# Optimization experiments

Hardware: AMD Instinct MI355X
Metric: run time of the kernel (lower is better)

Reference implementation:

```python
import jax, jax.numpy as jnp
import numpy as np

C = 128
IC = C // 2  # inter_channels
EPS = 1e-5   # InstanceNorm2d default eps (affine=False -> no learned scale/shift)


def setup_inputs() -> dict:
    key = jax.random.key(0)
    ks = jax.random.split(key, 9)
    s = 0.05
    return {
        "x": jax.random.normal(ks[0], (4, C, 64, 64), dtype=jnp.float32),
        "g_w": jax.random.normal(ks[1], (IC, C), dtype=jnp.float32) * s,
        "g_b": jax.random.normal(ks[2], (IC,), dtype=jnp.float32) * s,
        "theta_w": jax.random.normal(ks[3], (IC, C), dtype=jnp.float32) * s,
        "theta_b": jax.random.normal(ks[4], (IC,), dtype=jnp.float32) * s,
        "phi_w": jax.random.normal(ks[5], (IC, C), dtype=jnp.float32) * s,
        "phi_b": jax.random.normal(ks[6], (IC,), dtype=jnp.float32) * s,
        "W_w": jax.random.normal(ks[7], (C, IC), dtype=jnp.float32) * s,
        "W_b": jax.random.normal(ks[8], (C,), dtype=jnp.float32) * s,
    }


def reference(x, g_w, g_b, theta_w, theta_b, phi_w, phi_b, W_w, W_b):
    B, Cc, H, Wd = x.shape
    N = H * Wd
    xf = x.reshape(B, Cc, N)  # [B, C, N]

    def proj(w, b):  # 1x1 conv == channel matmul
        return jnp.einsum('oc,bcn->bon', w, xf) + b[:, None]  # [B, IC, N]

    g_x = proj(g_w, g_b).transpose(0, 2, 1)        # [B, N, IC]
    theta_x = proj(theta_w, theta_b).transpose(0, 2, 1)  # [B, N, IC]
    phi_x = proj(phi_w, phi_b)                     # [B, IC, N]

    f = jnp.einsum('bnc,bcm->bnm', theta_x, phi_x)  # [B, N, N] unscaled affinity
    f = jax.nn.softmax(f, axis=-1)
    y = jnp.einsum('bnm,bmc->bnc', f, g_x)          # [B, N, IC]
    y = y.transpose(0, 2, 1)                        # [B, IC, N]

    W_y = jnp.einsum('oc,bcn->bon', W_w, y) + W_b[:, None]  # [B, C, N]
    # InstanceNorm2d (affine=False): normalize per (batch, channel) over spatial
    mean = W_y.mean(axis=-1, keepdims=True)
    var = W_y.var(axis=-1, keepdims=True)
    W_y = (W_y - mean) * jax.lax.rsqrt(var + EPS)

    return x + W_y.reshape(B, Cc, H, Wd)
```

## Files before the change

### kernel.cpp

```cpp
#include <hip/hip_runtime.h>
#include <math.h>

typedef __attribute__((ext_vector_type(4))) float f32x4;
typedef __attribute__((ext_vector_type(8))) short s16x8;
typedef __attribute__((ext_vector_type(4))) short s16x4;
typedef __attribute__((ext_vector_type(4))) unsigned int u32x4;

#define NB 4
#define CH 128
#define ICH 64
#define NSP 4096
#define KSPLIT 16
#define SEGK (NSP / KSPLIT)
#define LDK 72
#define LDW 136

static __device__ __forceinline__ unsigned short f2bf(float f) {
  unsigned int u = __builtin_bit_cast(unsigned int, f);
  u += 0x7fffu + ((u >> 16) & 1u);
  return (unsigned short)(u >> 16);
}

__global__ __launch_bounds__(256) void k_proj(
    const float* __restrict__ x,
    const float* __restrict__ gw, const float* __restrict__ gbias,
    const float* __restrict__ tw, const float* __restrict__ tbias,
    const float* __restrict__ pw, const float* __restrict__ pbias,
    unsigned short* __restrict__ thetaT, unsigned short* __restrict__ phiT,
    unsigned short* __restrict__ gout)
{
  __shared__ __align__(16) float sxf[CH * 65];
  __shared__ __align__(16) unsigned short sW[ICH * LDW];
  const int b = blockIdx.y, z = blockIdx.z;
  const int n0 = blockIdx.x * 64;
  const int t = threadIdx.x;
  const float* Wz = (z == 0) ? tw : (z == 1) ? pw : gw;
  const float* Bz = (z == 0) ? tbias : (z == 1) ? pbias : gbias;
  const float scl = (z == 0) ? 1.44269504f : 1.0f;
  const float* xb = x + (size_t)b * CH * NSP;
#pragma unroll
  for (int i = 0; i < 8; ++i) {
    int idx = t + 256 * i;
    int c = idx >> 4, ch = idx & 15;
    *(float4*)(sxf + c * 65 + ch * 4) = *(const float4*)(xb + (size_t)c * NSP + n0 + ch * 4);
  }
#pragma unroll
  for (int i = 0; i < 8; ++i) {
    int idx = t + 256 * i;
    int o = idx >> 5, col = (idx & 31) * 4;
    float4 wv = *(const float4*)(Wz + o * CH + col);
    unsigned int p0 = (unsigned int)f2bf(wv.x) | ((unsigned int)f2bf(wv.y) << 16);
    unsigned int p1 = (unsigned int)f2bf(wv.z) | ((unsigned int)f2bf(wv.w) << 16);
    *(unsigned int*)(&sW[o * LDW + col]) = p0;
    *(unsigned int*)(&sW[o * LDW + col + 2]) = p1;
  }
  __syncthreads();

  const int wave = t >> 6, lane = t & 63;
  const int l15 = lane & 15, quad = lane >> 4;
  const int nw = wave * 16;
  s16x8 aq[4];
#pragma unroll
  for (int kc = 0; kc < 4; ++kc) {
#pragma unroll
    for (int j = 0; j < 8; ++j)
      aq[kc][j] = (short)f2bf(sxf[(kc * 32 + quad * 8 + j) * 65 + nw + l15]);
  }
  __syncthreads();

  unsigned short* ldsT = (unsigned short*)sxf;

#pragma unroll
  for (int osub = 0; osub < 4; ++osub) {
    f32x4 acc = (f32x4){0.f, 0.f, 0.f, 0.f};
#pragma unroll
    for (int kc = 0; kc < 4; ++kc) {
      const unsigned short* wp = &sW[(osub * 16 + l15) * LDW + kc * 32 + quad * 8];
      s16x4 lo = *(const s16x4*)(wp);
      s16x4 hi = *(const s16x4*)(wp + 4);
      s16x8 bw = __builtin_shufflevector(lo, hi, 0, 1, 2, 3, 4, 5, 6, 7);
      acc = __builtin_amdgcn_mfma_f32_16x16x32_bf16(aq[kc], bw, acc, 0, 0, 0);
    }
    float bv = Bz[osub * 16 + l15];
    if (z < 2) {
      unsigned short* outp = (z == 0) ? thetaT : phiT;
#pragma unroll
      for (int r = 0; r < 4; ++r)
        outp[((size_t)b * NSP + n0 + nw + quad * 4 + r) * ICH + osub * 16 + l15] =
            f2bf((acc[r] + bv) * scl);
    } else {
#pragma unroll
      for (int r = 0; r < 4; ++r)
        ldsT[(nw + quad * 4 + r) * LDK + osub * 16 + l15] = f2bf(acc[r] + bv);
    }
  }
  if (z == 2) {
    __syncthreads();
    int o = t >> 2, chunk = t & 3;
    unsigned short vv[16];
#pragma unroll
    for (int jj = 0; jj < 16; ++jj) vv[jj] = ldsT[(chunk * 16 + jj) * LDK + o];
    unsigned int words[8];
#pragma unroll
    for (int i = 0; i < 8; ++i)
      words[i] = (unsigned int)vv[2 * i] | ((unsigned int)vv[2 * i + 1] << 16);
    unsigned short* gp = gout + ((size_t)b * ICH + o) * NSP + n0 + chunk * 16;
    *(u32x4*)(gp) = (u32x4){words[0], words[1], words[2], words[3]};
    *(u32x4*)(gp + 8) = (u32x4){words[4], words[5], words[6], words[7]};
  }
}

__global__ __launch_bounds__(256, 2) void k_attn(
    const unsigned short* __restrict__ thetaT,
    const unsigned short* __restrict__ phiT,
    const unsigned short* __restrict__ gmat,
    unsigned short* __restrict__ Opart, float* __restrict__ lpart)
{
  __shared__ unsigned short ldsK[64 * LDK];
  __shared__ unsigned short ldsV[64 * LDK];
  __shared__ unsigned short ldsP[4][16 * LDK];
  const int qt = blockIdx.x, b = blockIdx.y, seg = blockIdx.z;
  const int t = threadIdx.x;
  const int wave = t >> 6, lane = t & 63;
  const int l15 = lane & 15, quad = lane >> 4;
  const int q0 = qt * 256 + wave * 64;

  s16x8 aq[4][2];
  const unsigned short* th = thetaT + ((size_t)b * NSP + q0) * ICH;
#pragma unroll
  for (int qs = 0; qs < 4; ++qs)
#pragma unroll
    for (int ks = 0; ks < 2; ++ks)
      aq[qs][ks] = __builtin_bit_cast(s16x8,
          *(const u32x4*)(th + (qs * 16 + l15) * ICH + ks * 32 + quad * 8));

  f32x4 Oacc[4][4];
  f32x4 lacc[4];
#pragma unroll
  for (int i = 0; i < 4; ++i) {
    lacc[i] = (f32x4){0.f, 0.f, 0.f, 0.f};
#pragma unroll
    for (int j = 0; j < 4; ++j) Oacc[i][j] = (f32x4){0.f, 0.f, 0.f, 0.f};
  }

  s16x8 bones;
  {
    short v = (l15 == 0) ? (short)0x3F80 : (short)0;
#pragma unroll
    for (int j = 0; j < 8; ++j) bones[j] = v;
  }

  const unsigned short* ph = phiT + (size_t)b * NSP * ICH;
  const unsigned short* gb = gmat + (size_t)b * ICH * NSP;
  const int k0 = seg * SEGK;

  for (int kt = 0; kt < SEGK / 64; ++kt) {
    const int key0 = k0 + kt * 64;
    __syncthreads();
#pragma unroll
    for (int i = 0; i < 4; ++i) {
      int idx = t + 256 * i;
      int rr = (idx >> 3) & 63, c8 = (idx & 7) * 8;
      if (idx < 512)
        *(u32x4*)(&ldsK[rr * LDK + c8]) =
            *(const u32x4*)(ph + (size_t)(key0 + rr) * ICH + c8);
      else
        *(u32x4*)(&ldsV[rr * LDK + c8]) =
            *(const u32x4*)(gb + (size_t)rr * NSP + key0 + c8);
    }
    __syncthreads();

    s16x8 bk[4][2];
#pragma unroll
    for (int kc = 0; kc < 4; ++kc)
#pragma unroll
      for (int ks = 0; ks < 2; ++ks)
        bk[kc][ks] = *(const s16x8*)(&ldsK[(kc * 16 + l15) * LDK + ks * 32 + quad * 8]);
    s16x8 bv[2][4];
#pragma unroll
    for (int ks = 0; ks < 2; ++ks)
#pragma unroll
      for (int ds = 0; ds < 4; ++ds)
        bv[ks][ds] = *(const s16x8*)(&ldsV[(ds * 16 + l15) * LDK + ks * 32 + quad * 8]);

    unsigned short* myP = &ldsP[wave][0];
#pragma unroll
    for (int qs = 0; qs < 4; ++qs) {
#pragma unroll
      for (int kc = 0; kc < 4; ++kc) {
        f32x4 sacc = (f32x4){0.f, 0.f, 0.f, 0.f};
        sacc = __builtin_amdgcn_mfma_f32_16x16x32_bf16(aq[qs][0], bk[kc][0], sacc, 0, 0, 0);
        sacc = __builtin_amdgcn_mfma_f32_16x16x32_bf16(aq[qs][1], bk[kc][1], sacc, 0, 0, 0);
#pragma unroll
        for (int r = 0; r < 4; ++r) {
          float e = exp2f(sacc[r]);
          myP[(quad * 4 + r) * LDK + kc * 16 + l15] =
              (unsigned short)(__builtin_bit_cast(unsigned int, e) >> 16);
        }
      }
#pragma unroll
      for (int ks = 0; ks < 2; ++ks) {
        s16x8 ap = *(const s16x8*)(&myP[l15 * LDK + ks * 32 + quad * 8]);
        lacc[qs] = __builtin_amdgcn_mfma_f32_16x16x32_bf16(ap, bones, lacc[qs], 0, 0, 0);
#pragma unroll
        for (int ds = 0; ds < 4; ++ds)
          Oacc[qs][ds] = __builtin_amdgcn_mfma_f32_16x16x32_bf16(ap, bv[ks][ds], Oacc[qs][ds], 0, 0, 0);
      }
    }
  }

  unsigned short* Ob = Opart + (((size_t)seg * NB + b) * NSP + q0) * ICH;
  unsigned short* myP = &ldsP[wave][0];
  const int erow = lane >> 3;
  const int ecol = (lane & 7) * 8;
#pragma unroll
  for (int qs = 0; qs < 4; ++qs) {
#pragma unroll
    for (int ds = 0; ds < 4; ++ds)
#pragma unroll
      for (int r = 0; r < 4; ++r)
        myP[(quad * 4 + r) * LDK + ds * 16 + l15] = f2bf(Oacc[qs][ds][r]);
    u32x4 w0 = *(const u32x4*)(&myP[erow * LDK + ecol]);
    u32x4 w1 = *(const u32x4*)(&myP[(8 + erow) * LDK + ecol]);
    *(u32x4*)(Ob + (qs * 16 + erow) * ICH + ecol) = w0;
    *(u32x4*)(Ob + (qs * 16 + 8 + erow) * ICH + ecol) = w1;
  }
  {
    float* myPf = (float*)myP;
    if (l15 == 0) {
#pragma unroll
      for (int qs = 0; qs < 4; ++qs)
#pragma unroll
        for (int r = 0; r < 4; ++r)
          myPf[qs * 16 + quad * 4 + r] = lacc[qs][r];
    }
    float* lb = lpart + ((size_t)seg * NB + b) * NSP + q0;
    lb[lane] = myPf[lane];
  }
}

__global__ __launch_bounds__(128) void k_wy(
    const unsigned short* __restrict__ Opart, const float* __restrict__ lpart,
    const float* __restrict__ Ww,
    float* __restrict__ WyT, float* __restrict__ stat)
{
  const int b = blockIdx.y, nt = blockIdx.x;
  const int t = threadIdx.x;
  const int wave = t >> 6, lane = t & 63;
  const int l15 = lane & 15, quad = lane >> 4;
  const int n0 = nt * 32 + wave * 16;
  float ls = 0.f;
#pragma unroll
  for (int s = 0; s < KSPLIT; ++s)
    ls += lpart[((size_t)s * NB + b) * NSP + n0 + l15];
  float inv = 1.0f / ls;
  s16x8 ay[2];
#pragma unroll
  for (int ks = 0; ks < 2; ++ks) {
    float acc8[8];
#pragma unroll
    for (int j = 0; j < 8; ++j) acc8[j] = 0.f;
#pragma unroll
    for (int s = 0; s < KSPLIT; ++s) {
      const unsigned short* op =
          Opart + (((size_t)s * NB + b) * NSP + n0 + l15) * ICH + ks * 32 + quad * 8;
      u32x4 raw = *(const u32x4*)op;
#pragma unroll
      for (int w2 = 0; w2 < 4; ++w2) {
        unsigned int u = raw[w2];
        acc8[2 * w2]     += __builtin_bit_cast(float, u << 16);
        acc8[2 * w2 + 1] += __builtin_bit_cast(float, u & 0xFFFF0000u);
      }
    }
#pragma unroll
    for (int j = 0; j < 8; ++j) ay[ks][j] = (short)f2bf(acc8[j] * inv);
  }
  s16x8 bw[8][2];
#pragma unroll
  for (int cc = 0; cc < 8; ++cc)
#pragma unroll
    for (int ks = 0; ks < 2; ++ks) {
      const float* wp = Ww + (cc * 16 + l15) * ICH + ks * 32 + quad * 8;
      s16x8 e;
#pragma unroll
      for (int j = 0; j < 8; ++j) e[j] = (short)f2bf(wp[j]);
      bw[cc][ks] = e;
    }
  float sums[8], sq[8];
#pragma unroll
  for (int cc = 0; cc < 8; ++cc) { sums[cc] = 0.f; sq[cc] = 0.f; }
#pragma unroll
  for (int cc = 0; cc < 8; ++cc) {
    f32x4 acc = (f32x4){0.f, 0.f, 0.f, 0.f};
    acc = __builtin_amdgcn_mfma_f32_16x16x32_bf16(ay[0], bw[cc][0], acc, 0, 0, 0);
    acc = __builtin_amdgcn_mfma_f32_16x16x32_bf16(ay[1], bw[cc][1], acc, 0, 0, 0);
    float* wout = WyT + ((size_t)b * NSP + n0 + quad * 4) * CH + cc * 16 + l15;
#pragma unroll
    for (int r = 0; r < 4; ++r) {
      float v = acc[r];
      sums[cc] += v;
      sq[cc] += v * v;
      wout[r * CH] = v;
    }
  }
#pragma unroll
  for (int cc = 0; cc < 8; ++cc) {
    sums[cc] += __shfl_xor(sums[cc], 16, 64);
    sums[cc] += __shfl_xor(sums[cc], 32, 64);
    sq[cc] += __shfl_xor(sq[cc], 16, 64);
    sq[cc] += __shfl_xor(sq[cc], 32, 64);
  }
  if (quad == 0) {
#pragma unroll
    for (int cc = 0; cc < 8; ++cc) {
      atomicAdd(&stat[(b * CH + cc * 16 + l15) * 2 + 0], sums[cc]);
      atomicAdd(&stat[(b * CH + cc * 16 + l15) * 2 + 1], sq[cc]);
    }
  }
}

__global__ __launch_bounds__(256) void k_norm(
    const float* __restrict__ WyT, const float* __restrict__ stat,
    const float* __restrict__ x, float* __restrict__ out)
{
  __shared__ float sWy[32 * 132];
  const int nt = blockIdx.x;
  const int b = blockIdx.y;
  const int t = threadIdx.x;
  const int n0 = nt * 32;
#pragma unroll
  for (int i = 0; i < 4; ++i) {
    int idx = t + 256 * i;
    int row = idx >> 5, c4 = idx & 31;
    *(float4*)(&sWy[row * 132 + c4 * 4]) =
        *(const float4*)(WyT + ((size_t)b * NSP + n0 + row) * CH + c4 * 4);
  }
  __syncthreads();
#pragma unroll
  for (int j = 0; j < 4; ++j) {
    int u = t + 256 * j;
    int co = u >> 3, nq = u & 7;
    float s = stat[(b * CH + co) * 2 + 0];
    float ss = stat[(b * CH + co) * 2 + 1];
    float mean = s * (1.f / NSP);
    float var = ss * (1.f / NSP) - mean * mean;
    float rs = rsqrtf(var + 1e-5f);
    float4 xv = *(const float4*)(x + (size_t)(b * CH + co) * NSP + n0 + nq * 4);
    float4 ov;
    ov.x = xv.x + (sWy[(nq * 4 + 0) * 132 + co] - mean) * rs;
    ov.y = xv.y + (sWy[(nq * 4 + 1) * 132 + co] - mean) * rs;
    ov.z = xv.z + (sWy[(nq * 4 + 2) * 132 + co] - mean) * rs;
    ov.w = xv.w + (sWy[(nq * 4 + 3) * 132 + co] - mean) * rs;
    *(float4*)(out + (size_t)(b * CH + co) * NSP + n0 + nq * 4) = ov;
  }
}

extern "C" void kernel_launch(void* const* d_in, const int* in_sizes, int n_in,
                              void* d_out, int out_size, void* d_ws, size_t ws_size,
                              hipStream_t stream)
{
  const float* x  = (const float*)d_in[0];
  const float* gw = (const float*)d_in[1];
  const float* gb = (const float*)d_in[2];
  const float* tw = (const float*)d_in[3];
  const float* tb = (const float*)d_in[4];
  const float* pw = (const float*)d_in[5];
  const float* pb = (const float*)d_in[6];
  const float* Ww = (const float*)d_in[7];
  float* out = (float*)d_out;
  char* ws = (char*)d_ws;
  unsigned short* thetaT = (unsigned short*)(ws);
  unsigned short* phiT   = (unsigned short*)(ws + (2ull << 20));
  unsigned short* gmat   = (unsigned short*)(ws + (4ull << 20));
  float* WyT   = (float*)(ws + (8ull << 20));
  float* stat  = (float*)(ws + (16ull << 20));
  float* lpart = (float*)(ws + (16ull << 20) + (1ull << 18));
  unsigned short* Opart = (unsigned short*)(ws + (17ull << 20) + (1ull << 18));

  hipMemsetAsync(stat, 0, NB * CH * 2 * sizeof(float), stream);
  k_proj<<<dim3(64, 4, 3), 256, 0, stream>>>(x, gw, gb, tw, tb, pw, pb, thetaT, phiT, gmat);
  k_attn<<<dim3(16, 4, KSPLIT), 256, 0, stream>>>(thetaT, phiT, gmat, Opart, lpart);
  k_wy<<<dim3(128, 4), 128, 0, stream>>>(Opart, lpart, Ww, WyT, stat);
  k_norm<<<dim3(128, 4), 256, 0, stream>>>(WyT, stat, x, out);
}
```

Measured before the change: 147.6 us.

## Pre-convert weights to bf16 once, fuse three projections per block, halve KSPLIT

Adds a small kernel that converts all four weight matrices to bf16 once and zeroes the stat buffer, replacing the memset. k_proj now computes theta, phi and g in one block per 32-column tile, reading x once instead of three times, and writes theta/phi through LDS as coalesced 16-byte stores. k_wy reads the pre-converted bf16 W weights directly. KSPLIT drops from 16 to 8, which halves the partial-output traffic in k_wy but reduces attention grid parallelism.

```diff
diff --git a/kernel.cpp b/kernel.cpp
--- a/kernel.cpp
+++ b/kernel.cpp
@@ -3,17 +3,16 @@
 
 typedef __attribute__((ext_vector_type(4))) float f32x4;
 typedef __attribute__((ext_vector_type(8))) short s16x8;
-typedef __attribute__((ext_vector_type(4))) short s16x4;
 typedef __attribute__((ext_vector_type(4))) unsigned int u32x4;
+typedef __attribute__((ext_vector_type(2))) unsigned int u32x2;
 
 #define NB 4
 #define CH 128
 #define ICH 64
 #define NSP 4096
-#define KSPLIT 16
+#define KSPLIT 8
 #define SEGK (NSP / KSPLIT)
 #define LDK 72
-#define LDW 136
 
 static __device__ __forceinline__ unsigned short f2bf(float f) {
   unsigned int u = __builtin_bit_cast(unsigned int, f);
@@ -21,92 +20,93 @@
   return (unsigned short)(u >> 16);
 }
 
-__global__ __launch_bounds__(256) void k_proj(
+__global__ __launch_bounds__(256) void k_wconv(
+    const float* __restrict__ tw, const float* __restrict__ pw,
+    const float* __restrict__ gw, const float* __restrict__ Ww,
+    unsigned short* __restrict__ Wwb, float* __restrict__ stat)
+{
+  int i = blockIdx.x * 256 + threadIdx.x;
+  int which = i >> 11;
+  const float* src = (which == 0) ? tw : (which == 1) ? pw : (which == 2) ? gw : Ww;
+  float4 v = ((const float4*)src)[i & 2047];
+  unsigned int p0 = (unsigned int)f2bf(v.x) | ((unsigned int)f2bf(v.y) << 16);
+  unsigned int p1 = (unsigned int)f2bf(v.z) | ((unsigned int)f2bf(v.w) << 16);
+  *(u32x2*)(Wwb + i * 4) = (u32x2){p0, p1};
+  if (blockIdx.x == 0) {
+    float4 z = {0.f, 0.f, 0.f, 0.f};
+    ((float4*)stat)[threadIdx.x] = z;
+  }
+}
+
+__global__ __launch_bounds__(128) void k_proj(
     const float* __restrict__ x,
-    const float* __restrict__ gw, const float* __restrict__ gbias,
-    const float* __restrict__ tw, const float* __restrict__ tbias,
-    const float* __restrict__ pw, const float* __restrict__ pbias,
+    const float* __restrict__ gbias, const float* __restrict__ tbias,
+    const float* __restrict__ pbias,
+    const unsigned short* __restrict__ Wwb,
     unsigned short* __restrict__ thetaT, unsigned short* __restrict__ phiT,
     unsigned short* __restrict__ gout)
 {
-  __shared__ __align__(16) float sxf[CH * 65];
-  __shared__ __align__(16) unsigned short sW[ICH * LDW];
-  const int b = blockIdx.y, z = blockIdx.z;
-  const int n0 = blockIdx.x * 64;
+  __shared__ __align__(16) unsigned short ldsT[32 * LDK];
+  const int b = blockIdx.y;
+  const int n0 = blockIdx.x * 32;
   const int t = threadIdx.x;
-  const float* Wz = (z == 0) ? tw : (z == 1) ? pw : gw;
-  const float* Bz = (z == 0) ? tbias : (z == 1) ? pbias : gbias;
-  const float scl = (z == 0) ? 1.44269504f : 1.0f;
-  const float* xb = x + (size_t)b * CH * NSP;
-#pragma unroll
-  for (int i = 0; i < 8; ++i) {
-    int idx = t + 256 * i;
-    int c = idx >> 4, ch = idx & 15;
-    *(float4*)(sxf + c * 65 + ch * 4) = *(const float4*)(xb + (size_t)c * NSP + n0 + ch * 4);
-  }
-#pragma unroll
-  for (int i = 0; i < 8; ++i) {
-    int idx = t + 256 * i;
-    int o = idx >> 5, col = (idx & 31) * 4;
-    float4 wv = *(const float4*)(Wz + o * CH + col);
-    unsigned int p0 = (unsigned int)f2bf(wv.x) | ((unsigned int)f2bf(wv.y) << 16);
-    unsigned int p1 = (unsigned int)f2bf(wv.z) | ((unsigned int)f2bf(wv.w) << 16);
-    *(unsigned int*)(&sW[o * LDW + col]) = p0;
-    *(unsigned int*)(&sW[o * LDW + col + 2]) = p1;
-  }
-  __syncthreads();
-
   const int wave = t >> 6, lane = t & 63;
   const int l15 = lane & 15, quad = lane >> 4;
-  const int nw = wave * 16;
+  const int n = n0 + wave * 16 + l15;
+  const float* xb = x + (size_t)b * CH * NSP;
+
   s16x8 aq[4];
 #pragma unroll
-  for (int kc = 0; kc < 4; ++kc) {
+  for (int kc = 0; kc < 4; ++kc)
 #pragma unroll
     for (int j = 0; j < 8; ++j)
-      aq[kc][j] = (short)f2bf(sxf[(kc * 32 + quad * 8 + j) * 65 + nw + l15]);
-  }
-  __syncthreads();
-
-  unsigned short* ldsT = (unsigned short*)sxf;
-
-#pragma unroll
-  for (int osub = 0; osub < 4; ++osub) {
-    f32x4 acc = (f32x4){0.f, 0.f, 0.f, 0.f};
-#pragma unroll
-    for (int kc = 0; kc < 4; ++kc) {
-      const unsigned short* wp = &sW[(osub * 16 + l15) * LDW + kc * 32 + quad * 8];
-      s16x4 lo = *(const s16x4*)(wp);
-      s16x4 hi = *(const s16x4*)(wp + 4);
-      s16x8 bw = __builtin_shufflevector(lo, hi, 0, 1, 2, 3, 4, 5, 6, 7);
-      acc = __builtin_amdgcn_mfma_f32_16x16x32_bf16(aq[kc], bw, acc, 0, 0, 0);
-    }
-    float bv = Bz[osub * 16 + l15];
+      aq[kc][j] = (short)f2bf(xb[(size_t)(kc * 32 + quad * 8 + j) * NSP + n]);
+
+  unsigned short* myT = &ldsT[wave * 16 * LDK];
+  const int erow = lane >> 3, ecol = (lane & 7) * 8;
+
+#pragma unroll
+  for (int z = 0; z < 3; ++z) {
+    const float* Bz = (z == 0) ? tbias : (z == 1) ? pbias : gbias;
+    const float scl = (z == 0) ? 1.44269504f : 1.0f;
+    const unsigned short* Wz = Wwb + z * (ICH * CH);
+#pragma unroll
+    for (int osub = 0; osub < 4; ++osub) {
+      f32x4 acc = (f32x4){0.f, 0.f, 0.f, 0.f};
+#pragma unroll
+      for (int kc = 0; kc < 4; ++kc) {
+        s16x8 bw = __builtin_bit_cast(s16x8,
+            *(const u32x4*)(Wz + (osub * 16 + l15) * CH + kc * 32 + quad * 8));
+        acc = __builtin_amdgcn_mfma_f32_16x16x32_bf16(aq[kc], bw, acc, 0, 0, 0);
+      }
+      float bv = Bz[osub * 16 + l15];
+#pragma unroll
+      for (int r = 0; r < 4; ++r)
+        myT[(quad * 4 + r) * LDK + osub * 16 + l15] = f2bf((acc[r] + bv) * scl);
+    }
     if (z < 2) {
-      unsigned short* outp = (z == 0) ? thetaT : phiT;
-#pragma unroll
-      for (int r = 0; r < 4; ++r)
-        outp[((size_t)b * NSP + n0 + nw + quad * 4 + r) * ICH + osub * 16 + l15] =
-            f2bf((acc[r] + bv) * scl);
+      unsigned short* outp = ((z == 0) ? thetaT : phiT) + ((size_t)b * NSP + n0 + wave * 16) * ICH;
+      u32x4 w0 = *(const u32x4*)(&myT[erow * LDK + ecol]);
+      u32x4 w1 = *(const u32x4*)(&myT[(8 + erow) * LDK + ecol]);
+      *(u32x4*)(outp + erow * ICH + ecol) = w0;
+      *(u32x4*)(outp + (8 + erow) * ICH + ecol) = w1;
     } else {
-#pragma unroll
-      for (int r = 0; r < 4; ++r)
-        ldsT[(nw + quad * 4 + r) * LDK + osub * 16 + l15] = f2bf(acc[r] + bv);
-    }
-  }
-  if (z == 2) {
-    __syncthreads();
-    int o = t >> 2, chunk = t & 3;
-    unsigned short vv[16];
-#pragma unroll
-    for (int jj = 0; jj < 16; ++jj) vv[jj] = ldsT[(chunk * 16 + jj) * LDK + o];
-    unsigned int words[8];
-#pragma unroll
-    for (int i = 0; i < 8; ++i)
-      words[i] = (unsigned int)vv[2 * i] | ((unsigned int)vv[2 * i + 1] << 16);
-    unsigned short* gp = gout + ((size_t)b * ICH + o) * NSP + n0 + chunk * 16;
-    *(u32x4*)(gp) = (u32x4){words[0], words[1], words[2], words[3]};
-    *(u32x4*)(gp + 8) = (u32x4){words[4], words[5], words[6], words[7]};
+      __syncthreads();
+#pragma unroll
+      for (int jj = 0; jj < 2; ++jj) {
+        int o = (wave * 2 + jj) * 16 + (lane >> 2);
+        int nch = (lane & 3) * 8;
+        unsigned short vv[8];
+#pragma unroll
+        for (int q2 = 0; q2 < 8; ++q2) vv[q2] = ldsT[(nch + q2) * LDK + o];
+        unsigned int words[4];
+#pragma unroll
+        for (int i2 = 0; i2 < 4; ++i2)
+          words[i2] = (unsigned int)vv[2 * i2] | ((unsigned int)vv[2 * i2 + 1] << 16);
+        *(u32x4*)(gout + ((size_t)b * ICH + o) * NSP + n0 + nch) =
+            (u32x4){words[0], words[1], words[2], words[3]};
+      }
+    }
   }
 }
 
@@ -241,7 +241,7 @@
 
 __global__ __launch_bounds__(128) void k_wy(
     const unsigned short* __restrict__ Opart, const float* __restrict__ lpart,
-    const float* __restrict__ Ww,
+    const unsigned short* __restrict__ Wwb,
     float* __restrict__ WyT, float* __restrict__ stat)
 {
   const int b = blockIdx.y, nt = blockIdx.x;
@@ -275,17 +275,14 @@
 #pragma unroll
     for (int j = 0; j < 8; ++j) ay[ks][j] = (short)f2bf(acc8[j] * inv);
   }
+  const unsigned short* Wb = Wwb + 3 * (ICH * CH);
   s16x8 bw[8][2];
 #pragma unroll
   for (int cc = 0; cc < 8; ++cc)
 #pragma unroll
-    for (int ks = 0; ks < 2; ++ks) {
-      const float* wp = Ww + (cc * 16 + l15) * ICH + ks * 32 + quad * 8;
-      s16x8 e;
-#pragma unroll
-      for (int j = 0; j < 8; ++j) e[j] = (short)f2bf(wp[j]);
-      bw[cc][ks] = e;
-    }
+    for (int ks = 0; ks < 2; ++ks)
+      bw[cc][ks] = __builtin_bit_cast(s16x8,
+          *(const u32x4*)(Wb + (cc * 16 + l15) * ICH + ks * 32 + quad * 8));
   float sums[8], sq[8];
 #pragma unroll
   for (int cc = 0; cc < 8; ++cc) { sums[cc] = 0.f; sq[cc] = 0.f; }
@@ -374,12 +371,13 @@
   unsigned short* gmat   = (unsigned short*)(ws + (4ull << 20));
   float* WyT   = (float*)(ws + (8ull << 20));
   float* stat  = (float*)(ws + (16ull << 20));
-  float* lpart = (float*)(ws + (16ull << 20) + (1ull << 18));
-  unsigned short* Opart = (unsigned short*)(ws + (17ull << 20) + (1ull << 18));
-
-  hipMemsetAsync(stat, 0, NB * CH * 2 * sizeof(float), stream);
-  k_proj<<<dim3(64, 4, 3), 256, 0, stream>>>(x, gw, gb, tw, tb, pw, pb, thetaT, phiT, gmat);
+  unsigned short* Wwb = (unsigned short*)(ws + (16ull << 20) + 65536);
+  float* lpart = (float*)(ws + (16ull << 20) + (1ull << 19));
+  unsigned short* Opart = (unsigned short*)(ws + (17ull << 20));
+
+  k_wconv<<<dim3(32), 256, 0, stream>>>(tw, pw, gw, Ww, Wwb, stat);
+  k_proj<<<dim3(128, 4), 128, 0, stream>>>(x, gb, tb, pb, Wwb, thetaT, phiT, gmat);
   k_attn<<<dim3(16, 4, KSPLIT), 256, 0, stream>>>(thetaT, phiT, gmat, Opart, lpart);
-  k_wy<<<dim3(128, 4), 128, 0, stream>>>(Opart, lpart, Ww, WyT, stat);
+  k_wy<<<dim3(128, 4), 128, 0, stream>>>(Opart, lpart, Wwb, WyT, stat);
   k_norm<<<dim3(128, 4), 256, 0, stream>>>(WyT, stat, x, out);
 }
```

New measurement: 142.2 us. 1.04x faster.
